# Performance work log

Measured on AMD Instinct MI355X. Metric: run time of the kernel, lower is better.

## Reference

```python
import jax, jax.numpy as jnp
import numpy as np

B, T, D, H = 2, 2048, 1024, 16
DH = D // H

def setup_inputs() -> dict:
    key = jax.random.key(0)
    ks = jax.random.split(key, 5)
    scale = 1.0 / np.sqrt(D)
    x = jax.random.normal(ks[0], (B, T, D), dtype=jnp.float32)
    Wq = jax.random.normal(ks[1], (D, D), dtype=jnp.float32) * scale
    Wk = jax.random.normal(ks[2], (D, D), dtype=jnp.float32) * scale
    Wv = jax.random.normal(ks[3], (D, D), dtype=jnp.float32) * scale
    Wo = jax.random.normal(ks[4], (D, D), dtype=jnp.float32) * scale
    # causal mask: True means masked (matches torch masked_fill semantics)
    mask = jnp.triu(jnp.ones((T, T), dtype=bool), k=1)
    return {"x": x, "mask": mask, "Wq": Wq, "Wk": Wk, "Wv": Wv, "Wo": Wo}

def reference(x, mask, Wq, Wk, Wv, Wo):
    b, t, c = x.shape
    # projections -> [B, H, T, DH]
    def split_heads(y):
        return y.reshape(b, t, H, DH).transpose(0, 2, 1, 3)
    q = split_heads(x @ Wq)
    k = split_heads(x @ Wk)
    v = split_heads(x @ Wv)
    # scores [B, H, T, T]
    att = jnp.einsum('bhqd,bhkd->bhqk', q, k) / jnp.sqrt(jnp.float32(DH))
    att = jnp.where(mask, -jnp.inf, att)
    att = jax.nn.softmax(att, axis=-1)
    # dropout=0.0 (eval-mode determinism)
    out = jnp.einsum('bhqk,bhkd->bhqd', att, v)
    out = out.transpose(0, 2, 1, 3).reshape(b, t, c)
    return out @ Wo
```

## Files before the change

### kernel.cpp

```cpp
#include <hip/hip_runtime.h>
#include <stdint.h>

typedef unsigned short u16;
typedef unsigned int u32;
typedef __attribute__((ext_vector_type(8))) short s16x8;
typedef __attribute__((ext_vector_type(4))) float f32x4;
typedef __attribute__((ext_vector_type(8))) unsigned short u16x8;
typedef __attribute__((ext_vector_type(4))) unsigned short u16x4;

#define T_ 2048
#define D_ 1024
#define H_ 16
#define DH_ 64

#define QSCALE_LOG2E 0.18033688011112042f

#if __has_builtin(__builtin_amdgcn_exp2f)
#define EXP2(x) __builtin_amdgcn_exp2f(x)
#else
#define EXP2(x) exp2f(x)
#endif

__device__ __forceinline__ float bf2f(u16 u) {
    union { unsigned int i; float f; } x; x.i = ((unsigned int)u) << 16; return x.f;
}
__device__ __forceinline__ u16 f2bf(float f) {
    union { float f; unsigned int i; } x; x.f = f;
    unsigned int u = x.i;
    u += 0x7fffu + ((u >> 16) & 1u);
    return (u16)(u >> 16);
}
#if __has_builtin(__builtin_amdgcn_cvt_pk_bf16_f32)
__device__ __forceinline__ u32 pack_rn(float a, float b) {
    typedef __attribute__((ext_vector_type(2))) __bf16 bf16x2_t;
    bf16x2_t r = __builtin_amdgcn_cvt_pk_bf16_f32(a, b);
    union { bf16x2_t v; u32 u; } x; x.v = r; return x.u;
}
#else
__device__ __forceinline__ u32 pack_rn(float a, float b) {
    union { float f; u32 u; } ua, ub; ua.f = a; ub.f = b;
    return ((ua.u + 0x8000u) >> 16) | ((ub.u + 0x8000u) & 0xffff0000u);
}
#endif

__device__ __forceinline__ void gload16(const u16* g, u16* l) {
    __builtin_amdgcn_global_load_lds(
        (const __attribute__((address_space(1))) void*)g,
        (__attribute__((address_space(3))) void*)l,
        16, 0, 0);
}

__global__ __launch_bounds__(256) void prep_kernel(const float* __restrict__ x,
                                                   const float* __restrict__ Wq,
                                                   const float* __restrict__ Wk,
                                                   const float* __restrict__ Wv,
                                                   const float* __restrict__ Wo,
                                                   u16* __restrict__ xb,
                                                   u16* __restrict__ WT) {
    __shared__ float tile[32][33];
    int blk = blockIdx.x;
    if (blk < 4096) {
        int i = (blk * 256 + threadIdx.x) * 4;
        float4 v = *(const float4*)(x + i);
        u16x4 o;
        o[0] = f2bf(v.x); o[1] = f2bf(v.y); o[2] = f2bf(v.z); o[3] = f2bf(v.w);
        *(u16x4*)(xb + i) = o;
    } else {
        int t = blk - 4096;
        int s = t >> 10;
        const float* W = (s == 0) ? Wq : (s == 1) ? Wk : (s == 2) ? Wv : Wo;
        int n0 = ((t >> 5) & 31) * 32;
        int k0 = (t & 31) * 32;
        int tx = threadIdx.x & 31, ty = threadIdx.x >> 5;
        #pragma unroll
        for (int j = 0; j < 32; j += 8)
            tile[ty + j][tx] = W[(k0 + ty + j) * D_ + n0 + tx];
        __syncthreads();
        u16* dst = WT + (size_t)s * D_ * D_;
        #pragma unroll
        for (int j = 0; j < 32; j += 8)
            dst[(n0 + ty + j) * D_ + k0 + tx] = f2bf(tile[tx][ty + j]);
    }
}

__global__ __launch_bounds__(256) void gemm_qkv(const u16* __restrict__ A,
                                                const u16* __restrict__ Bt,
                                                u16* __restrict__ Qw,
                                                u16* __restrict__ Kw,
                                                u16* __restrict__ Vw) {
    __shared__ __align__(16) u16 As[2][128 * 32];
    __shared__ __align__(16) u16 Bs[2][128 * 32];
    const int m0 = blockIdx.x * 128, n0 = blockIdx.y * 128;
    int tid = threadIdx.x;
    int w = tid >> 6, lane = tid & 63, quad = lane >> 4, l15 = lane & 15;
    int wr = w >> 1, wc = w & 1;

    int nb0 = (w << 7), nb1 = nb0 + 64;
    int c0 = nb0 + lane, c1 = nb1 + lane;
    int r0 = c0 >> 2, k0off = (((c0 & 3) ^ ((r0 >> 1) & 3)) << 3);
    int r1 = c1 >> 2, k1off = (((c1 & 3) ^ ((r1 >> 1) & 3)) << 3);
    const u16* Ar0 = A + (size_t)(m0 + r0) * D_ + k0off;
    const u16* Ar1 = A + (size_t)(m0 + r1) * D_ + k1off;
    const u16* Br0 = Bt + (size_t)(n0 + r0) * D_ + k0off;
    const u16* Br1 = Bt + (size_t)(n0 + r1) * D_ + k1off;

    f32x4 acc[4][4];
    #pragma unroll
    for (int mi = 0; mi < 4; ++mi)
        #pragma unroll
        for (int ni = 0; ni < 4; ++ni) acc[mi][ni] = (f32x4){0.f, 0.f, 0.f, 0.f};

    gload16(Ar0, &As[0][nb0 << 3]);
    gload16(Ar1, &As[0][nb1 << 3]);
    gload16(Br0, &Bs[0][nb0 << 3]);
    gload16(Br1, &Bs[0][nb1 << 3]);

    for (int k0 = 0; k0 < D_; k0 += 32) {
        int buf = (k0 >> 5) & 1;
        __syncthreads();
        if (k0 + 32 < D_) {
            int kn = k0 + 32;
            gload16(Ar0 + kn, &As[buf ^ 1][nb0 << 3]);
            gload16(Ar1 + kn, &As[buf ^ 1][nb1 << 3]);
            gload16(Br0 + kn, &Bs[buf ^ 1][nb0 << 3]);
            gload16(Br1 + kn, &Bs[buf ^ 1][nb1 << 3]);
        }
        s16x8 af[4], bf[4];
        #pragma unroll
        for (int mi = 0; mi < 4; ++mi) {
            int R = wr * 64 + mi * 16 + l15;
            af[mi] = *(const s16x8*)&As[buf][((R << 2) | (quad ^ ((R >> 1) & 3))) << 3];
        }
        #pragma unroll
        for (int ni = 0; ni < 4; ++ni) {
            int R = wc * 64 + ni * 16 + l15;
            bf[ni] = *(const s16x8*)&Bs[buf][((R << 2) | (quad ^ ((R >> 1) & 3))) << 3];
        }
        #pragma unroll
        for (int mi = 0; mi < 4; ++mi)
            #pragma unroll
            for (int ni = 0; ni < 4; ++ni)
                acc[mi][ni] = __builtin_amdgcn_mfma_f32_16x16x32_bf16(af[mi], bf[ni],
                                                                      acc[mi][ni], 0, 0, 0);
    }

    #pragma unroll
    for (int mi = 0; mi < 4; ++mi) {
        int mbase = m0 + wr * 64 + mi * 16 + quad * 4;
        #pragma unroll
        for (int ni = 0; ni < 4; ++ni) {
            int n = n0 + wc * 64 + ni * 16 + l15;
            int b = mbase >> 11, t0 = mbase & 2047;
            int sel = n >> 10, nn = n & 1023;
            int h = nn >> 6, dh = nn & 63;
            int bhidx = (b << 4) + h;
            if (sel == 0) {
                #pragma unroll
                for (int r = 0; r < 4; ++r)
                    Qw[(size_t)(bhidx * T_ + t0 + r) * DH_ + dh] =
                        f2bf(acc[mi][ni][r] * QSCALE_LOG2E);
            } else if (sel == 1) {
                #pragma unroll
                for (int r = 0; r < 4; ++r)
                    Kw[(size_t)(bhidx * T_ + t0 + r) * DH_ + dh] = f2bf(acc[mi][ni][r]);
            } else {
                uint2 pk;
                pk.x = pack_rn(acc[mi][ni][0], acc[mi][ni][1]);
                pk.y = pack_rn(acc[mi][ni][2], acc[mi][ni][3]);
                *(uint2*)(Vw + ((size_t)bhidx * DH_ + dh) * T_ + t0) = pk;
            }
        }
    }
}

__global__ __launch_bounds__(256) void gemm_out(const u16* __restrict__ A,
                                                const u16* __restrict__ Bt,
                                                float* __restrict__ Cout) {
    __shared__ __align__(16) u16 As[2][128 * 32];
    __shared__ __align__(16) u16 Bs[2][64 * 32];
    const int m0 = blockIdx.x * 128, n0 = blockIdx.y * 64;
    int tid = threadIdx.x;
    int w = tid >> 6, lane = tid & 63, quad = lane >> 4, l15 = lane & 15;

    int nbA0 = (w << 7), nbA1 = nbA0 + 64, nbB = (w << 6);
    int cA0 = nbA0 + lane, cA1 = nbA1 + lane, cB = nbB + lane;
    int rA0 = cA0 >> 2, kA0 = (((cA0 & 3) ^ ((rA0 >> 1) & 3)) << 3);
    int rA1 = cA1 >> 2, kA1 = (((cA1 & 3) ^ ((rA1 >> 1) & 3)) << 3);
    int rB  = cB >> 2,  kB  = (((cB  & 3) ^ ((rB  >> 1) & 3)) << 3);
    const u16* ArA0 = A + (size_t)(m0 + rA0) * D_ + kA0;
    const u16* ArA1 = A + (size_t)(m0 + rA1) * D_ + kA1;
    const u16* BrB  = Bt + (size_t)(n0 + rB) * D_ + kB;

    f32x4 acc[2][4];
    #pragma unroll
    for (int mi = 0; mi < 2; ++mi)
        #pragma unroll
        for (int ni = 0; ni < 4; ++ni) acc[mi][ni] = (f32x4){0.f, 0.f, 0.f, 0.f};

    gload16(ArA0, &As[0][nbA0 << 3]);
    gload16(ArA1, &As[0][nbA1 << 3]);
    gload16(BrB,  &Bs[0][nbB << 3]);

    for (int k0 = 0; k0 < D_; k0 += 32) {
        int buf = (k0 >> 5) & 1;
        __syncthreads();
        if (k0 + 32 < D_) {
            int kn = k0 + 32;
            gload16(ArA0 + kn, &As[buf ^ 1][nbA0 << 3]);
            gload16(ArA1 + kn, &As[buf ^ 1][nbA1 << 3]);
            gload16(BrB + kn,  &Bs[buf ^ 1][nbB << 3]);
        }
        s16x8 af[2], bf[4];
        #pragma unroll
        for (int mi = 0; mi < 2; ++mi) {
            int R = w * 32 + mi * 16 + l15;
            af[mi] = *(const s16x8*)&As[buf][((R << 2) | (quad ^ ((R >> 1) & 3))) << 3];
        }
        #pragma unroll
        for (int ni = 0; ni < 4; ++ni) {
            int R = ni * 16 + l15;
            bf[ni] = *(const s16x8*)&Bs[buf][((R << 2) | (quad ^ ((R >> 1) & 3))) << 3];
        }
        #pragma unroll
        for (int mi = 0; mi < 2; ++mi)
            #pragma unroll
            for (int ni = 0; ni < 4; ++ni)
                acc[mi][ni] = __builtin_amdgcn_mfma_f32_16x16x32_bf16(af[mi], bf[ni],
                                                                      acc[mi][ni], 0, 0, 0);
    }

    #pragma unroll
    for (int mi = 0; mi < 2; ++mi) {
        int mbase = m0 + w * 32 + mi * 16 + quad * 4;
        #pragma unroll
        for (int ni = 0; ni < 4; ++ni) {
            int n = n0 + ni * 16 + l15;
            #pragma unroll
            for (int r = 0; r < 4; ++r)
                Cout[(size_t)(mbase + r) * D_ + n] = acc[mi][ni][r];
        }
    }
}

__global__ __launch_bounds__(256) void attn_mfma_kernel(const u16* __restrict__ Qg,
                                                        const u16* __restrict__ Kg,
                                                        const u16* __restrict__ Vt,
                                                        u16* __restrict__ Opart,
                                                        float* __restrict__ lpart) {
    __shared__ __align__(16) u16 Kbuf[2][64 * 64];
    __shared__ __align__(16) u16 Vbuf[2][64 * 64];
    __shared__ __align__(16) u16 Ps[4][16 * 64];

    int blk = blockIdx.x;
    int xcd = blk & 7, slot = blk >> 3;
    int bh = (xcd << 2) + (slot / 40);
    int x  = slot % 40;
    int BX, c;
    if (x < 4)       { BX = x;                    c = 0; }
    else if (x < 12) { BX = 4 + ((x - 4) >> 1);   c = (x - 4) & 1; }
    else if (x < 24) { BX = 8 + (x - 12) / 3;     c = (x - 12) % 3; }
    else             { BX = 12 + ((x - 24) >> 2); c = (x - 24) & 3; }
    int kstart = c << 3;
    int ktm = 2 * BX + 1;
    int kend = min(kstart + 8, ktm + 1);

    int tid = threadIdx.x;
    int w = tid >> 6, lane = tid & 63, quad = lane >> 4, l15 = lane & 15;
    int q0 = BX << 7;
    int qA = q0 + 16 * w;
    int qB = q0 + 64 + 16 * w;

    const u16* Qb = Qg + (size_t)bh * T_ * DH_;
    const u16* Kb = Kg + (size_t)bh * T_ * DH_;
    const u16* Vb = Vt + (size_t)bh * DH_ * T_;

    s16x8 qa0 = *(const s16x8*)(Qb + (size_t)(qA + l15) * DH_ + quad * 8);
    s16x8 qa1 = *(const s16x8*)(Qb + (size_t)(qA + l15) * DH_ + quad * 8 + 32);
    s16x8 qc0 = *(const s16x8*)(Qb + (size_t)(qB + l15) * DH_ + quad * 8);
    s16x8 qc1 = *(const s16x8*)(Qb + (size_t)(qB + l15) * DH_ + quad * 8 + 32);

    int nb0 = (w << 7), nb1 = nb0 + 64;
    int n0c = nb0 + lane, n1c = nb1 + lane;
    int r0 = n0c >> 3, c0s = n0c & 7, g0 = (r0 << 3) + (c0s ^ (r0 & 7));
    int r1 = n1c >> 3, c1s = n1c & 7, g1 = (r1 << 3) + (c1s ^ (r1 & 7));

    int pbase = l15 << 6;
    int psw = l15 & 7;
    u16* PsW = Ps[w];

    {
        int kb0 = kstart << 6;
        const u16* Ktile = Kb + (size_t)kb0 * DH_;
        gload16(Ktile + (g0 << 3), &Kbuf[0][nb0 << 3]);
        gload16(Ktile + (g1 << 3), &Kbuf[0][nb1 << 3]);
        gload16(Vb + (size_t)r0 * T_ + kb0 + ((g0 & 7) << 3), &Vbuf[0][nb0 << 3]);
        gload16(Vb + (size_t)r1 * T_ + kb0 + ((g1 & 7) << 3), &Vbuf[0][nb1 << 3]);
    }

    f32x4 oA[4] = {{0.f,0.f,0.f,0.f},{0.f,0.f,0.f,0.f},{0.f,0.f,0.f,0.f},{0.f,0.f,0.f,0.f}};
    f32x4 oB[4] = {{0.f,0.f,0.f,0.f},{0.f,0.f,0.f,0.f},{0.f,0.f,0.f,0.f},{0.f,0.f,0.f,0.f}};
    f32x4 lAv = {0.f,0.f,0.f,0.f}, lBv = {0.f,0.f,0.f,0.f};

    for (int kt = kstart; kt < kend; ++kt) {
        int buf = (kt - kstart) & 1;
        __syncthreads();

        if (kt + 1 < kend) {
            int kb2 = (kt + 1) << 6;
            const u16* Ktile = Kb + (size_t)kb2 * DH_;
            gload16(Ktile + (g0 << 3), &Kbuf[buf ^ 1][nb0 << 3]);
            gload16(Ktile + (g1 << 3), &Kbuf[buf ^ 1][nb1 << 3]);
            gload16(Vb + (size_t)r0 * T_ + kb2 + ((g0 & 7) << 3), &Vbuf[buf ^ 1][nb0 << 3]);
            gload16(Vb + (size_t)r1 * T_ + kb2 + ((g1 & 7) << 3), &Vbuf[buf ^ 1][nb1 << 3]);
        }

        f32x4 sA[4], sB[4];
        #pragma unroll
        for (int g = 0; g < 4; ++g) {
            int r = (g << 4) + l15;
            int cc = quad ^ (r & 7);
            s16x8 ka0 = *(const s16x8*)&Kbuf[buf][((r << 3) + cc) << 3];
            s16x8 ka1 = *(const s16x8*)&Kbuf[buf][((r << 3) + (cc ^ 4)) << 3];
            f32x4 z = {0.f, 0.f, 0.f, 0.f};
            sA[g] = __builtin_amdgcn_mfma_f32_16x16x32_bf16(ka0, qa0, z, 0, 0, 0);
            sA[g] = __builtin_amdgcn_mfma_f32_16x16x32_bf16(ka1, qa1, sA[g], 0, 0, 0);
            sB[g] = __builtin_amdgcn_mfma_f32_16x16x32_bf16(ka0, qc0, z, 0, 0, 0);
            sB[g] = __builtin_amdgcn_mfma_f32_16x16x32_bf16(ka1, qc1, sB[g], 0, 0, 0);
        }

        if (kt >= ktm - 1) {
            int rA = q0 + 16 * w + l15 - (kt << 6);
            #pragma unroll
            for (int g = 0; g < 4; ++g)
                #pragma unroll
                for (int r = 0; r < 4; ++r)
                    if ((g << 4) + (quad << 2) + r > rA) sA[g][r] = -INFINITY;
        }
        if (kt == ktm) {
            int rB = 16 * w + l15;
            #pragma unroll
            for (int g = 0; g < 4; ++g)
                #pragma unroll
                for (int r = 0; r < 4; ++r)
                    if ((g << 4) + (quad << 2) + r > rB) sB[g][r] = -INFINITY;
        }

        #pragma unroll
        for (int g = 0; g < 4; ++g)
            #pragma unroll
            for (int r = 0; r < 4; ++r) {
                float pA = EXP2(sA[g][r]); sA[g][r] = pA; lAv[r] += pA;
                float pB = EXP2(sB[g][r]); sB[g][r] = pB; lBv[r] += pB;
            }

        #pragma unroll
        for (int g = 0; g < 4; ++g) {
            uint2 pk;
            pk.x = pack_rn(sA[g][0], sA[g][1]); pk.y = pack_rn(sA[g][2], sA[g][3]);
            int cs = ((g << 1) | (quad >> 1)) ^ psw;
            *(uint2*)&PsW[pbase + (cs << 3) + ((quad & 1) << 2)] = pk;
        }
        int rc = quad ^ psw;
        s16x8 pa0 = *(const s16x8*)&PsW[pbase + (rc << 3)];
        s16x8 pa1 = *(const s16x8*)&PsW[pbase + ((rc ^ 4) << 3)];
        #pragma unroll
        for (int g = 0; g < 4; ++g) {
            uint2 pk;
            pk.x = pack_rn(sB[g][0], sB[g][1]); pk.y = pack_rn(sB[g][2], sB[g][3]);
            int cs = ((g << 1) | (quad >> 1)) ^ psw;
            *(uint2*)&PsW[pbase + (cs << 3) + ((quad & 1) << 2)] = pk;
        }
        s16x8 pc0 = *(const s16x8*)&PsW[pbase + (rc << 3)];
        s16x8 pc1 = *(const s16x8*)&PsW[pbase + ((rc ^ 4) << 3)];

        #pragma unroll
        for (int g = 0; g < 4; ++g) {
            int r = (g << 4) + l15;
            int cc = quad ^ (r & 7);
            s16x8 va0 = *(const s16x8*)&Vbuf[buf][((r << 3) + cc) << 3];
            s16x8 va1 = *(const s16x8*)&Vbuf[buf][((r << 3) + (cc ^ 4)) << 3];
            oA[g] = __builtin_amdgcn_mfma_f32_16x16x32_bf16(va0, pa0, oA[g], 0, 0, 0);
            oA[g] = __builtin_amdgcn_mfma_f32_16x16x32_bf16(va1, pa1, oA[g], 0, 0, 0);
            oB[g] = __builtin_amdgcn_mfma_f32_16x16x32_bf16(va0, pc0, oB[g], 0, 0, 0);
            oB[g] = __builtin_amdgcn_mfma_f32_16x16x32_bf16(va1, pc1, oB[g], 0, 0, 0);
        }
    }

    float lA = (lAv[0] + lAv[1]) + (lAv[2] + lAv[3]);
    float lB = (lBv[0] + lBv[1]) + (lBv[2] + lBv[3]);
    lA += __shfl_xor(lA, 16); lA += __shfl_xor(lA, 32);
    lB += __shfl_xor(lB, 16); lB += __shfl_xor(lB, 32);
    int slotid = ((bh << 4) + BX) * 4 + c;
    u16* dA = Opart + ((size_t)slotid * 128 + 16 * w + l15) * 64;
    u16* dB = dA + 64 * 64;
    #pragma unroll
    for (int g = 0; g < 4; ++g) {
        uint2 pk;
        pk.x = pack_rn(oA[g][0], oA[g][1]); pk.y = pack_rn(oA[g][2], oA[g][3]);
        *(uint2*)(dA + (g << 4) + (quad << 2)) = pk;
        pk.x = pack_rn(oB[g][0], oB[g][1]); pk.y = pack_rn(oB[g][2], oB[g][3]);
        *(uint2*)(dB + (g << 4) + (quad << 2)) = pk;
    }
    if (quad == 0) {
        lpart[(size_t)slotid * 128 + 16 * w + l15] = lA;
        lpart[(size_t)slotid * 128 + 64 + 16 * w + l15] = lB;
    }
}

__global__ __launch_bounds__(256) void reduce_attn(const u16* __restrict__ Opart,
                                                   const float* __restrict__ lpart,
                                                   u16* __restrict__ att) {
    int BX = blockIdx.x, bh = blockIdx.y;
    int nch = (BX >> 2) + 1;
    int tid = threadIdx.x;
    int row = tid >> 1, dh0 = (tid & 1) << 5;
    int slotbase = ((bh << 4) + BX) << 2;

    float acc[32];
    #pragma unroll
    for (int i = 0; i < 32; ++i) acc[i] = 0.f;
    float l = 0.f;
    for (int cc = 0; cc < nch; ++cc) {
        const u16* op = Opart + ((size_t)(slotbase + cc) * 128 + row) * 64 + dh0;
        #pragma unroll
        for (int v = 0; v < 4; ++v) {
            u16x8 o8 = *(const u16x8*)(op + v * 8);
            #pragma unroll
            for (int j = 0; j < 8; ++j) acc[v * 8 + j] += bf2f(o8[j]);
        }
        l += lpart[(size_t)(slotbase + cc) * 128 + row];
    }
    float inv = 1.f / l;
    int b = bh >> 4, h = bh & 15;
    int q = (BX << 7) + row;
    u16* dst = att + ((size_t)(b * T_) + q) * D_ + (h << 6) + dh0;
    #pragma unroll
    for (int v = 0; v < 4; ++v) {
        u16x8 o8;
        #pragma unroll
        for (int j = 0; j < 8; ++j) o8[j] = f2bf(acc[v * 8 + j] * inv);
        *(u16x8*)(dst + v * 8) = o8;
    }
}

extern "C" void kernel_launch(void* const* d_in, const int* in_sizes, int n_in,
                              void* d_out, int out_size, void* d_ws, size_t ws_size,
                              hipStream_t stream) {
    const float* x  = (const float*)d_in[0];
    const float* Wq = (const float*)d_in[2];
    const float* Wk = (const float*)d_in[3];
    const float* Wv = (const float*)d_in[4];
    const float* Wo = (const float*)d_in[5];
    float* out = (float*)d_out;

    char* ws = (char*)d_ws;
    u16*   xb    = (u16*)(ws);
    u16*   WT    = (u16*)(ws + (8ull  << 20));
    u16*   Qw    = (u16*)(ws + (16ull << 20));
    u16*   Kw    = (u16*)(ws + (24ull << 20));
    u16*   Vw    = (u16*)(ws + (32ull << 20));
    u16*   att   = (u16*)(ws + (40ull << 20));
    u16*   Opart = (u16*)(ws + (48ull << 20));
    float* lpart = (float*)(ws + (82ull << 20));

    prep_kernel<<<dim3(8192), dim3(256), 0, stream>>>(x, Wq, Wk, Wv, Wo, xb, WT);
    gemm_qkv<<<dim3(32, 24), dim3(256), 0, stream>>>(xb, WT, Qw, Kw, Vw);
    attn_mfma_kernel<<<dim3(1280), dim3(256), 0, stream>>>(Qw, Kw, Vw, Opart, lpart);
    reduce_attn<<<dim3(16, 32), dim3(256), 0, stream>>>(Opart, lpart, att);
    gemm_out<<<dim3(32, 16), dim3(256), 0, stream>>>(att, WT + 3ull * 1048576ull, out);
}
```

Measured before the change: 195.8 us.

## Fuse x bf16 conversion into QKV GEMM and split-K the output projection

The separate fp32-to-bf16 conversion of x is removed from the prep kernel. gemm_qkv now loads fp32 x directly, packs it to bf16 in registers and writes it into swizzled LDS, which saves a full write and read of the bf16 copy. The output GEMM is split along K into two halves that accumulate into a zeroed output with float atomics, doubling block count for better occupancy. The cost is a memset, atomic traffic, run-to-run nondeterminism in the fp32 sums, and synchronous register-staged A loads in place of async global-to-LDS loads.

After: 259.4 us. +32.5%, slower.

```diff
diff --git a/kernel.cpp b/kernel.cpp
--- a/kernel.cpp
+++ b/kernel.cpp
@@ -50,40 +50,29 @@
         16, 0, 0);
 }
 
-__global__ __launch_bounds__(256) void prep_kernel(const float* __restrict__ x,
-                                                   const float* __restrict__ Wq,
-                                                   const float* __restrict__ Wk,
-                                                   const float* __restrict__ Wv,
-                                                   const float* __restrict__ Wo,
-                                                   u16* __restrict__ xb,
-                                                   u16* __restrict__ WT) {
+__global__ __launch_bounds__(256) void prep_w_kernel(const float* __restrict__ Wq,
+                                                     const float* __restrict__ Wk,
+                                                     const float* __restrict__ Wv,
+                                                     const float* __restrict__ Wo,
+                                                     u16* __restrict__ WT) {
     __shared__ float tile[32][33];
-    int blk = blockIdx.x;
-    if (blk < 4096) {
-        int i = (blk * 256 + threadIdx.x) * 4;
-        float4 v = *(const float4*)(x + i);
-        u16x4 o;
-        o[0] = f2bf(v.x); o[1] = f2bf(v.y); o[2] = f2bf(v.z); o[3] = f2bf(v.w);
-        *(u16x4*)(xb + i) = o;
-    } else {
-        int t = blk - 4096;
-        int s = t >> 10;
-        const float* W = (s == 0) ? Wq : (s == 1) ? Wk : (s == 2) ? Wv : Wo;
-        int n0 = ((t >> 5) & 31) * 32;
-        int k0 = (t & 31) * 32;
-        int tx = threadIdx.x & 31, ty = threadIdx.x >> 5;
-        #pragma unroll
-        for (int j = 0; j < 32; j += 8)
-            tile[ty + j][tx] = W[(k0 + ty + j) * D_ + n0 + tx];
-        __syncthreads();
-        u16* dst = WT + (size_t)s * D_ * D_;
-        #pragma unroll
-        for (int j = 0; j < 32; j += 8)
-            dst[(n0 + ty + j) * D_ + k0 + tx] = f2bf(tile[tx][ty + j]);
-    }
-}
-
-__global__ __launch_bounds__(256) void gemm_qkv(const u16* __restrict__ A,
+    int t = blockIdx.x;
+    int s = t >> 10;
+    const float* W = (s == 0) ? Wq : (s == 1) ? Wk : (s == 2) ? Wv : Wo;
+    int n0 = ((t >> 5) & 31) * 32;
+    int k0 = (t & 31) * 32;
+    int tx = threadIdx.x & 31, ty = threadIdx.x >> 5;
+    #pragma unroll
+    for (int j = 0; j < 32; j += 8)
+        tile[ty + j][tx] = W[(k0 + ty + j) * D_ + n0 + tx];
+    __syncthreads();
+    u16* dst = WT + (size_t)s * D_ * D_;
+    #pragma unroll
+    for (int j = 0; j < 32; j += 8)
+        dst[(n0 + ty + j) * D_ + k0 + tx] = f2bf(tile[tx][ty + j]);
+}
+
+__global__ __launch_bounds__(256) void gemm_qkv(const float* __restrict__ X,
                                                 const u16* __restrict__ Bt,
                                                 u16* __restrict__ Qw,
                                                 u16* __restrict__ Kw,
@@ -95,12 +84,17 @@
     int w = tid >> 6, lane = tid & 63, quad = lane >> 4, l15 = lane & 15;
     int wr = w >> 1, wc = w & 1;
 
+    int arow = tid >> 1, acol = (tid & 1) << 4;
+    const float* Axp = X + (size_t)(m0 + arow) * D_ + acol;
+    int asw = (arow >> 1) & 3;
+    int ac0 = (tid & 1) << 1;
+    int as0 = (arow << 2) | (ac0 ^ asw);
+    int as1 = (arow << 2) | ((ac0 | 1) ^ asw);
+
     int nb0 = (w << 7), nb1 = nb0 + 64;
     int c0 = nb0 + lane, c1 = nb1 + lane;
     int r0 = c0 >> 2, k0off = (((c0 & 3) ^ ((r0 >> 1) & 3)) << 3);
     int r1 = c1 >> 2, k1off = (((c1 & 3) ^ ((r1 >> 1) & 3)) << 3);
-    const u16* Ar0 = A + (size_t)(m0 + r0) * D_ + k0off;
-    const u16* Ar1 = A + (size_t)(m0 + r1) * D_ + k1off;
     const u16* Br0 = Bt + (size_t)(n0 + r0) * D_ + k0off;
     const u16* Br1 = Bt + (size_t)(n0 + r1) * D_ + k1off;
 
@@ -110,8 +104,19 @@
         #pragma unroll
         for (int ni = 0; ni < 4; ++ni) acc[mi][ni] = (f32x4){0.f, 0.f, 0.f, 0.f};
 
-    gload16(Ar0, &As[0][nb0 << 3]);
-    gload16(Ar1, &As[0][nb1 << 3]);
+    {
+        float4 a0 = *(const float4*)(Axp + 0);
+        float4 a1 = *(const float4*)(Axp + 4);
+        float4 a2 = *(const float4*)(Axp + 8);
+        float4 a3 = *(const float4*)(Axp + 12);
+        union { u32 wd[4]; u16x8 v; } P0, P1;
+        P0.wd[0] = pack_rn(a0.x, a0.y); P0.wd[1] = pack_rn(a0.z, a0.w);
+        P0.wd[2] = pack_rn(a1.x, a1.y); P0.wd[3] = pack_rn(a1.z, a1.w);
+        P1.wd[0] = pack_rn(a2.x, a2.y); P1.wd[1] = pack_rn(a2.z, a2.w);
+        P1.wd[2] = pack_rn(a3.x, a3.y); P1.wd[3] = pack_rn(a3.z, a3.w);
+        *(u16x8*)&As[0][as0 << 3] = P0.v;
+        *(u16x8*)&As[0][as1 << 3] = P1.v;
+    }
     gload16(Br0, &Bs[0][nb0 << 3]);
     gload16(Br1, &Bs[0][nb1 << 3]);
 
@@ -120,10 +125,19 @@
         __syncthreads();
         if (k0 + 32 < D_) {
             int kn = k0 + 32;
-            gload16(Ar0 + kn, &As[buf ^ 1][nb0 << 3]);
-            gload16(Ar1 + kn, &As[buf ^ 1][nb1 << 3]);
+            float4 a0 = *(const float4*)(Axp + kn);
+            float4 a1 = *(const float4*)(Axp + kn + 4);
+            float4 a2 = *(const float4*)(Axp + kn + 8);
+            float4 a3 = *(const float4*)(Axp + kn + 12);
             gload16(Br0 + kn, &Bs[buf ^ 1][nb0 << 3]);
             gload16(Br1 + kn, &Bs[buf ^ 1][nb1 << 3]);
+            union { u32 wd[4]; u16x8 v; } P0, P1;
+            P0.wd[0] = pack_rn(a0.x, a0.y); P0.wd[1] = pack_rn(a0.z, a0.w);
+            P0.wd[2] = pack_rn(a1.x, a1.y); P0.wd[3] = pack_rn(a1.z, a1.w);
+            P1.wd[0] = pack_rn(a2.x, a2.y); P1.wd[1] = pack_rn(a2.z, a2.w);
+            P1.wd[2] = pack_rn(a3.x, a3.y); P1.wd[3] = pack_rn(a3.z, a3.w);
+            *(u16x8*)&As[buf ^ 1][as0 << 3] = P0.v;
+            *(u16x8*)&As[buf ^ 1][as1 << 3] = P1.v;
         }
         s16x8 af[4], bf[4];
         #pragma unroll
@@ -179,6 +193,7 @@
     __shared__ __align__(16) u16 As[2][128 * 32];
     __shared__ __align__(16) u16 Bs[2][64 * 32];
     const int m0 = blockIdx.x * 128, n0 = blockIdx.y * 64;
+    const int koff = blockIdx.z * 512;
     int tid = threadIdx.x;
     int w = tid >> 6, lane = tid & 63, quad = lane >> 4, l15 = lane & 15;
 
@@ -187,9 +202,9 @@
     int rA0 = cA0 >> 2, kA0 = (((cA0 & 3) ^ ((rA0 >> 1) & 3)) << 3);
     int rA1 = cA1 >> 2, kA1 = (((cA1 & 3) ^ ((rA1 >> 1) & 3)) << 3);
     int rB  = cB >> 2,  kB  = (((cB  & 3) ^ ((rB  >> 1) & 3)) << 3);
-    const u16* ArA0 = A + (size_t)(m0 + rA0) * D_ + kA0;
-    const u16* ArA1 = A + (size_t)(m0 + rA1) * D_ + kA1;
-    const u16* BrB  = Bt + (size_t)(n0 + rB) * D_ + kB;
+    const u16* ArA0 = A + (size_t)(m0 + rA0) * D_ + koff + kA0;
+    const u16* ArA1 = A + (size_t)(m0 + rA1) * D_ + koff + kA1;
+    const u16* BrB  = Bt + (size_t)(n0 + rB) * D_ + koff + kB;
 
     f32x4 acc[2][4];
     #pragma unroll
@@ -201,10 +216,10 @@
     gload16(ArA1, &As[0][nbA1 << 3]);
     gload16(BrB,  &Bs[0][nbB << 3]);
 
-    for (int k0 = 0; k0 < D_; k0 += 32) {
+    for (int k0 = 0; k0 < 512; k0 += 32) {
         int buf = (k0 >> 5) & 1;
         __syncthreads();
-        if (k0 + 32 < D_) {
+        if (k0 + 32 < 512) {
             int kn = k0 + 32;
             gload16(ArA0 + kn, &As[buf ^ 1][nbA0 << 3]);
             gload16(ArA1 + kn, &As[buf ^ 1][nbA1 << 3]);
@@ -237,7 +252,7 @@
             int n = n0 + ni * 16 + l15;
             #pragma unroll
             for (int r = 0; r < 4; ++r)
-                Cout[(size_t)(mbase + r) * D_ + n] = acc[mi][ni][r];
+                atomicAdd(&Cout[(size_t)(mbase + r) * D_ + n], acc[mi][ni][r]);
         }
     }
 }
@@ -454,18 +469,18 @@
     float* out = (float*)d_out;
 
     char* ws = (char*)d_ws;
-    u16*   xb    = (u16*)(ws);
-    u16*   WT    = (u16*)(ws + (8ull  << 20));
-    u16*   Qw    = (u16*)(ws + (16ull << 20));
-    u16*   Kw    = (u16*)(ws + (24ull << 20));
-    u16*   Vw    = (u16*)(ws + (32ull << 20));
-    u16*   att   = (u16*)(ws + (40ull << 20));
-    u16*   Opart = (u16*)(ws + (48ull << 20));
-    float* lpart = (float*)(ws + (82ull << 20));
-
-    prep_kernel<<<dim3(8192), dim3(256), 0, stream>>>(x, Wq, Wk, Wv, Wo, xb, WT);
-    gemm_qkv<<<dim3(32, 24), dim3(256), 0, stream>>>(xb, WT, Qw, Kw, Vw);
+    u16*   WT    = (u16*)(ws);
+    u16*   Qw    = (u16*)(ws + (8ull  << 20));
+    u16*   Kw    = (u16*)(ws + (16ull << 20));
+    u16*   Vw    = (u16*)(ws + (24ull << 20));
+    u16*   att   = (u16*)(ws + (32ull << 20));
+    u16*   Opart = (u16*)(ws + (40ull << 20));
+    float* lpart = (float*)(ws + (74ull << 20));
+
+    hipMemsetAsync(d_out, 0, (size_t)out_size * sizeof(float), stream);
+    prep_w_kernel<<<dim3(4096), dim3(256), 0, stream>>>(Wq, Wk, Wv, Wo, WT);
+    gemm_qkv<<<dim3(32, 24), dim3(256), 0, stream>>>(x, WT, Qw, Kw, Vw);
     attn_mfma_kernel<<<dim3(1280), dim3(256), 0, stream>>>(Qw, Kw, Vw, Opart, lpart);
     reduce_attn<<<dim3(16, 32), dim3(256), 0, stream>>>(Opart, lpart, att);
-    gemm_out<<<dim3(32, 16), dim3(256), 0, stream>>>(att, WT + 3ull * 1048576ull, out);
-}
+    gemm_out<<<dim3(32, 16, 2), dim3(256), 0, stream>>>(att, WT + 3ull * 1048576ull, out);
+}
```
